# Optimization experiments

Hardware: AMD Instinct MI355X
Metric: run time of the kernel (lower is better)

## Reference

```python
import jax, jax.numpy as jnp
import numpy as np

B, S, D, E, F = 2, 2048, 1024, 14, 2048


def setup_inputs() -> dict:
    key = jax.random.key(0)
    k = jax.random.split(key, 4)
    h = jax.random.normal(k[0], (B, S, D), dtype=jnp.float32)
    router_w = jax.random.normal(k[1], (D, E), dtype=jnp.float32) * 0.02
    # kaiming-uniform-like scale for expert weights
    w1 = jax.random.uniform(k[2], (E, D, F), dtype=jnp.float32,
                            minval=-1.0, maxval=1.0) * float(np.sqrt(6.0 / D))
    w2 = jax.random.uniform(k[3], (E, F, D), dtype=jnp.float32,
                            minval=-1.0, maxval=1.0) * float(np.sqrt(6.0 / F))
    b1 = jnp.zeros((E, F), dtype=jnp.float32)
    b2 = jnp.zeros((E, D), dtype=jnp.float32)
    return {"h": h, "router_w": router_w, "w1": w1, "b1": b1, "w2": w2, "b2": b2}


def reference(h, router_w, w1, b1, w2, b2):
    Bb, Ss, Dd = h.shape
    x = h.reshape(-1, Dd)                                  # (N, D)
    logits = x @ router_w                                  # (N, E)
    assignments = jnp.argmax(logits, axis=-1)              # (N,) phase B routing
    probs = jax.nn.softmax(logits, axis=-1)
    weights = jnp.take_along_axis(probs, assignments[:, None], axis=1)[:, 0]  # (N,)
    # dense all-expert FFN (as in the original module)
    hid = jnp.einsum('nd,edf->nef', x, w1) + b1            # (N, E, F)
    hid = jax.nn.gelu(hid, approximate=False)
    all_out = jnp.einsum('nef,efd->ned', hid, w2) + b2     # (N, E, D)
    sel = jnp.take_along_axis(all_out, assignments[:, None, None], axis=1)[:, 0, :]
    moe_out = (sel * weights[:, None]).reshape(Bb, Ss, Dd)
    return moe_out
```

## Files before the change

kernel.cpp:

```cpp
#include <hip/hip_runtime.h>
#include <hip/hip_bf16.h>


#define NTOK 4096
#define NEXP 14
#define DDIM 1024
#define FDIM 2048

typedef __attribute__((ext_vector_type(8))) short short8;
typedef __attribute__((ext_vector_type(4))) float floatx4;

__device__ __forceinline__ unsigned bfr(float f) {
  unsigned u = __float_as_uint(f);
  return (u + 0x7FFFu + ((u >> 16) & 1u)) >> 16;
}
__device__ __forceinline__ unsigned pk2(float a, float b) {
  return bfr(a) | (bfr(b) << 16);
}

__device__ __forceinline__ void gload16(const void* g, void* l) {
  __builtin_amdgcn_global_load_lds((const __attribute__((address_space(1))) void*)g,
                                   (__attribute__((address_space(3))) void*)l, 16, 0, 0);
}

__global__ void k_init(const float* __restrict__ rw, float* __restrict__ rwT) {
  int i = blockIdx.x * 256 + threadIdx.x;
  if (i < DDIM * NEXP) rwT[(i % NEXP) * DDIM + i / NEXP] = rw[i];
}

__global__ __launch_bounds__(256) void k_router(
    const float* __restrict__ x, const float* __restrict__ rwT,
    int* __restrict__ assign, float* __restrict__ wgt,
    unsigned short* __restrict__ h16) {
  int wid = threadIdx.x >> 6, lane = threadIdx.x & 63;
  int n = blockIdx.x * 4 + wid;
  const float* xr = x + (size_t)n * DDIM;
  unsigned short* hr = h16 + (size_t)n * DDIM;
  double acc[NEXP];
#pragma unroll
  for (int e = 0; e < NEXP; e++) acc[e] = 0.0;
#pragma unroll
  for (int i = 0; i < 4; i++) {
    int d0 = i * 256 + lane * 4;
    float4 xv = *(const float4*)(xr + d0);
    uint2 hb;
    hb.x = pk2(xv.x, xv.y);
    hb.y = pk2(xv.z, xv.w);
    *(uint2*)(hr + d0) = hb;
    double x0 = xv.x, x1 = xv.y, x2 = xv.z, x3 = xv.w;
#pragma unroll
    for (int e = 0; e < NEXP; e++) {
      float4 rv = *(const float4*)(rwT + e * DDIM + d0);
      acc[e] += x0 * (double)rv.x + x1 * (double)rv.y + x2 * (double)rv.z + x3 * (double)rv.w;
    }
  }
#pragma unroll
  for (int e = 0; e < NEXP; e++)
    for (int m = 32; m > 0; m >>= 1) acc[e] += __shfl_xor(acc[e], m, 64);
  int best = 0;
  double bv = acc[0];
#pragma unroll
  for (int e = 1; e < NEXP; e++)
    if (acc[e] > bv) { bv = acc[e]; best = e; }
  float s = 0.f;
#pragma unroll
  for (int e = 0; e < NEXP; e++) s += expf((float)(acc[e] - bv));
  if (lane == 0) {
    wgt[n] = 1.0f / s;
    assign[n] = best;
  }
}

__global__ __launch_bounds__(1024) void k_sort(
    const int* __restrict__ assign, int* __restrict__ cnt,
    int* __restrict__ list, int* __restrict__ tiles, int* __restrict__ ntl) {
  __shared__ int clds[64][NEXP];
  __shared__ int tot[16];
  __shared__ int tstart[NEXP + 1];
  int tid = threadIdx.x;
  int wv = tid >> 6, lane = tid & 63;
  unsigned long long below = (1ull << lane) - 1ull;
  int e4[4], r4[4];
#pragma unroll
  for (int t = 0; t < 4; t++) {
    int n = wv * 256 + t * 64 + lane;
    int e = assign[n];
    int rank = 0, gcnt = 0;
#pragma unroll
    for (int xx = 0; xx < NEXP; xx++) {
      unsigned long long m = __ballot(e == xx);
      if (e == xx) rank = __popcll(m & below);
      if (lane == xx) gcnt = __popcll(m);
    }
    e4[t] = e;
    r4[t] = rank;
    if (lane < NEXP) clds[wv * 4 + t][lane] = gcnt;
  }
  __syncthreads();
  if (wv < NEXP) {
    int v = clds[lane][wv];
    int s = v;
    for (int m = 1; m < 64; m <<= 1) {
      int t = __shfl_up(s, m, 64);
      if (lane >= m) s += t;
    }
    clds[lane][wv] = s - v;
    if (lane == 63) {
      cnt[wv] = s;
      tot[wv] = s;
    }
  }
  __syncthreads();
#pragma unroll
  for (int t = 0; t < 4; t++) {
    int n = wv * 256 + t * 64 + lane;
    int e = e4[t];
    int pos = clds[wv * 4 + t][e] + r4[t];
    list[e * NTOK + pos] = n;
  }
  if (wv == 15) {
    int c = (lane < NEXP) ? tot[lane] : 0;
    int nt = (c + 127) >> 7;
    int st = nt;
    for (int m = 1; m < 64; m <<= 1) {
      int t = __shfl_up(st, m, 64);
      if (lane >= m) st += t;
    }
    if (lane < NEXP) tstart[lane] = st - nt;
    if (lane == NEXP - 1) {
      tstart[NEXP] = st;
      *ntl = st;
    }
    int totT = __shfl(st, NEXP - 1, 64);
    if (lane < totT) {
      int e = 0;
      while (tstart[e + 1] <= lane) e++;
      tiles[2 * lane] = e;
      tiles[2 * lane + 1] = (lane - tstart[e]) * 128;
    }
  }
}

__global__ __launch_bounds__(256) void k_prep(const float* __restrict__ W,
                                              unsigned short* __restrict__ img,
                                              int K, int N) {
  __shared__ float t32[4096];
  int KB = K >> 6, NB = N >> 6, K4 = KB >> 2;
  int b = blockIdx.x;
  int kb4 = b % K4;
  int nb_ = b / K4;
  int nblk = nb_ % NB, e = nb_ / NB;
  int t = threadIdx.x;
  int k = t >> 4, n4 = (t & 15) * 4;
  for (int z = 0; z < 4; z++) {
    int kblk = kb4 * 4 + z;
    const float* src = W + (size_t)e * K * N + (size_t)(kblk * 64) * N + nblk * 64;
#pragma unroll
    for (int j = 0; j < 4; j++) {
      int kk = k + j * 16;
      float4 v = *(const float4*)(src + (size_t)kk * N + n4);
      int sw = kk & 31;
      t32[kk * 64 + ((n4 + 0) ^ sw)] = v.x;
      t32[kk * 64 + ((n4 + 1) ^ sw)] = v.y;
      t32[kk * 64 + ((n4 + 2) ^ sw)] = v.z;
      t32[kk * 64 + ((n4 + 3) ^ sw)] = v.w;
    }
    __syncthreads();
    unsigned short* dst = img + (size_t)((e * NB + nblk) * KB + kblk) * 4096;
#pragma unroll
    for (int c = 0; c < 2; c++) {
      int ci = t + c * 256;
      int col = ci >> 3, q = ci & 7, k8 = q ^ (col & 7);
      float f[8];
#pragma unroll
      for (int j = 0; j < 8; j++) {
        int kk = k8 * 8 + j;
        f[j] = t32[kk * 64 + (col ^ (kk & 31))];
      }
      uint4 o;
      o.x = pk2(f[0], f[1]);
      o.y = pk2(f[2], f[3]);
      o.z = pk2(f[4], f[5]);
      o.w = pk2(f[6], f[7]);
      *(uint4*)(dst + ci * 8) = o;
    }
    __syncthreads();
  }
}

template <int LAYER>
__global__ __launch_bounds__(256, 3) void k_gemm_img(
    const unsigned short* __restrict__ Xb, const unsigned short* __restrict__ img,
    const float* __restrict__ Bias, const float* __restrict__ wgt,
    unsigned short* __restrict__ outB, float* __restrict__ outF,
    const int* __restrict__ wsI, const int* __restrict__ list) {
  constexpr int K = (LAYER == 1) ? DDIM : FDIM;
  constexpr int N = (LAYER == 1) ? FDIM : DDIM;
  constexpr int NIT = K / 64;
  constexpr int KB = K / 64, NB = N / 64;

  const int* cnt = wsI;
  const int* ntl = wsI + 48;
  const int* tiles = wsI + 64;

  int tI = blockIdx.y;
  if (tI >= *ntl) return;
  int e = tiles[2 * tI], m0 = tiles[2 * tI + 1];
  int rows = cnt[e] - m0;
  int base = e * NTOK + m0;
  int n0 = blockIdx.x * 64;

  __shared__ char sA[2][16384];
  __shared__ char sB[2][8192];
  __shared__ int tokL[128];
  __shared__ float wgtL[128];

  int tid = threadIdx.x;
  if (tid < 128) {
    int tok = list[base + tid] & (NTOK - 1);
    tokL[tid] = tok;
    if (LAYER == 2) wgtL[tid] = wgt[tok];
  }
  __syncthreads();

  int lane = tid & 63, wid = tid >> 6, wm = wid >> 1, wn = wid & 1;

  const char* gA[4];
  {
    unsigned sw = (unsigned)(((lane & 7) * 16) ^ ((lane >> 3) << 4));
#pragma unroll
    for (int j = 0; j < 4; j++) {
      int row = wid * 32 + j * 8 + (lane >> 3);
      gA[j] = (const char*)(Xb + (size_t)tokL[row] * K) + sw;
    }
  }
  const char* gB = (const char*)img +
                   (size_t)((e * NB + (n0 >> 6)) * KB) * 8192 + wid * 2048 + lane * 16;

  floatx4 acc[4][2];
#pragma unroll
  for (int i = 0; i < 4; i++)
#pragma unroll
    for (int j = 0; j < 2; j++) acc[i][j] = (floatx4){0.f, 0.f, 0.f, 0.f};

#define GLOAD_AB(it, p)                                                     \
  do {                                                                      \
    _Pragma("unroll") for (int j = 0; j < 4; j++)                           \
        gload16(gA[j] + (size_t)(it) * 128, sA[p] + (wid * 4 + j) * 1024);  \
    _Pragma("unroll") for (int j = 0; j < 2; j++)                           \
        gload16(gB + (size_t)(it) * 8192 + j * 1024,                        \
                sB[p] + wid * 2048 + j * 1024);                             \
  } while (0)

#define MFMA_PHASE(P)                                                                    \
  do {                                                                                   \
    const char* A_ = sA[P];                                                              \
    const char* B_ = sB[P];                                                              \
    _Pragma("unroll") for (int kc = 0; kc < 2; kc++) {                                   \
      short8 af[4], bf[2];                                                               \
      int kb = kc * 64 + ((lane >> 4) << 4);                                             \
      _Pragma("unroll") for (int f = 0; f < 4; f++) {                                    \
        int rr = wm * 64 + f * 16 + (lane & 15);                                         \
        af[f] = *(const short8*)(A_ + rr * 128 + (kb ^ ((rr & 7) << 4)));                \
      }                                                                                  \
      _Pragma("unroll") for (int f = 0; f < 2; f++) {                                    \
        int cc = wn * 32 + f * 16 + (lane & 15);                                         \
        bf[f] = *(const short8*)(B_ + cc * 128 + (kb ^ ((cc & 7) << 4)));                \
      }                                                                                  \
      _Pragma("unroll") for (int fm = 0; fm < 4; fm++)                                   \
      _Pragma("unroll") for (int fn = 0; fn < 2; fn++)                                   \
          acc[fm][fn] =                                                                  \
              __builtin_amdgcn_mfma_f32_16x16x32_bf16(af[fm], bf[fn], acc[fm][fn], 0, 0, 0); \
    }                                                                                    \
  } while (0)

  GLOAD_AB(0, 0);
  for (int it = 0; it < NIT - 1; ++it) {
    int p = it & 1;
    __builtin_amdgcn_sched_barrier(0);
    __builtin_amdgcn_s_barrier();
    GLOAD_AB(it + 1, p ^ 1);
    __builtin_amdgcn_sched_barrier(0);
    asm volatile("s_waitcnt vmcnt(6)" ::: "memory");
    __builtin_amdgcn_s_barrier();
    __builtin_amdgcn_sched_barrier(0);
    MFMA_PHASE(p);
  }
  {
    int p = (NIT - 1) & 1;
    __builtin_amdgcn_sched_barrier(0);
    __builtin_amdgcn_s_barrier();
    asm volatile("s_waitcnt vmcnt(0)" ::: "memory");
    __builtin_amdgcn_s_barrier();
    __builtin_amdgcn_sched_barrier(0);
    MFMA_PHASE(p);
  }
#undef GLOAD_AB
#undef MFMA_PHASE

  float bv[2];
#pragma unroll
  for (int f = 0; f < 2; f++) bv[f] = Bias[(size_t)e * N + n0 + wn * 32 + f * 16 + (lane & 15)];
#pragma unroll
  for (int fm = 0; fm < 4; fm++) {
#pragma unroll
    for (int r = 0; r < 4; r++) {
      int gr = wm * 64 + fm * 16 + ((lane >> 4) << 2) + r;
      if (gr < rows) {
        int tok = tokL[gr];
#pragma unroll
        for (int fn = 0; fn < 2; fn++) {
          int col = n0 + wn * 32 + fn * 16 + (lane & 15);
          float v = acc[fm][fn][r] + bv[fn];
          if (LAYER == 1) {
            v = 0.5f * v * (1.0f + erff(v * 0.70710678118654752f));
            outB[(size_t)tok * FDIM + col] = (unsigned short)bfr(v);
          } else {
            outF[(size_t)tok * DDIM + col] = v * wgtL[gr];
          }
        }
      }
    }
  }
}

extern "C" void kernel_launch(void* const* d_in, const int* in_sizes, int n_in,
                              void* d_out, int out_size, void* d_ws, size_t ws_size,
                              hipStream_t stream) {
  const float* h  = (const float*)d_in[0];
  const float* rw = (const float*)d_in[1];
  const float* w1 = (const float*)d_in[2];
  const float* b1 = (const float*)d_in[3];
  const float* w2 = (const float*)d_in[4];
  const float* b2 = (const float*)d_in[5];
  float* out = (float*)d_out;

  int* wsI = (int*)d_ws;
  int* assign = wsI + 160;
  float* wgt = (float*)(wsI + 4256);
  int* list = (int*)((char*)d_ws + 65536);
  float* rwT = (float*)((char*)d_ws + 294912);
  unsigned short* hid  = (unsigned short*)((char*)d_ws + 393216);
  unsigned short* h16  = (unsigned short*)((char*)d_ws + 17170432);
  unsigned short* img1 = (unsigned short*)((char*)d_ws + 25559040);
  unsigned short* img2 = (unsigned short*)((char*)d_ws + 17170432);

  k_init<<<56, 256, 0, stream>>>(rw, rwT);
  k_router<<<NTOK / 4, 256, 0, stream>>>(h, rwT, assign, wgt, h16);
  k_sort<<<1, 1024, 0, stream>>>(assign, wsI, list, wsI + 64, wsI + 48);
  k_prep<<<NEXP * (FDIM / 64) * (DDIM / 64 / 4), 256, 0, stream>>>(w1, img1, DDIM, FDIM);
  k_gemm_img<1><<<dim3(FDIM / 64, 45), 256, 0, stream>>>(h16, img1, b1, nullptr, hid, nullptr, wsI, list);
  k_prep<<<NEXP * (DDIM / 64) * (FDIM / 64 / 4), 256, 0, stream>>>(w2, img2, FDIM, DDIM);
  k_gemm_img<2><<<dim3(DDIM / 64, 45), 256, 0, stream>>>(hid, img2, b2, wgt, nullptr, out, wsI, list);
}
```

Baseline: 188.6 us.

## Co-schedule weight prep with router and layer-1 GEMM via fused launches

Merges the w1 bf16 image prep into the router launch and the w2 image prep into the layer-1 GEMM launch, using block-index ranges to dispatch each block to one body. The aim is to overlap the bandwidth-bound weight conversion with other work and to cut the number of launches. img2 moves to its own workspace region so it no longer aliases h16 while layer 1 still reads h16. In exchange the fused kernels carry the larger shared-memory footprint and the GEMM's register budget, which can lower occupancy for the prep blocks.

```diff
diff --git a/kernel.cpp b/kernel.cpp
--- a/kernel.cpp
+++ b/kernel.cpp
@@ -23,17 +23,28 @@
                                    (__attribute__((address_space(3))) void*)l, 16, 0, 0);
 }
 
+struct GemmSh {
+  char sA[2][16384];
+  char sB[2][8192];
+  int tokL[128];
+  float wgtL[128];
+};
+union FuseSh {
+  GemmSh g;
+  float t32[4096];
+};
+
 __global__ void k_init(const float* __restrict__ rw, float* __restrict__ rwT) {
   int i = blockIdx.x * 256 + threadIdx.x;
   if (i < DDIM * NEXP) rwT[(i % NEXP) * DDIM + i / NEXP] = rw[i];
 }
 
-__global__ __launch_bounds__(256) void k_router(
-    const float* __restrict__ x, const float* __restrict__ rwT,
+__device__ __forceinline__ void router_body(
+    int bid, const float* __restrict__ x, const float* __restrict__ rwT,
     int* __restrict__ assign, float* __restrict__ wgt,
     unsigned short* __restrict__ h16) {
   int wid = threadIdx.x >> 6, lane = threadIdx.x & 63;
-  int n = blockIdx.x * 4 + wid;
+  int n = bid * 4 + wid;
   const float* xr = x + (size_t)n * DDIM;
   unsigned short* hr = h16 + (size_t)n * DDIM;
   double acc[NEXP];
@@ -71,82 +82,11 @@
   }
 }
 
-__global__ __launch_bounds__(1024) void k_sort(
-    const int* __restrict__ assign, int* __restrict__ cnt,
-    int* __restrict__ list, int* __restrict__ tiles, int* __restrict__ ntl) {
-  __shared__ int clds[64][NEXP];
-  __shared__ int tot[16];
-  __shared__ int tstart[NEXP + 1];
-  int tid = threadIdx.x;
-  int wv = tid >> 6, lane = tid & 63;
-  unsigned long long below = (1ull << lane) - 1ull;
-  int e4[4], r4[4];
-#pragma unroll
-  for (int t = 0; t < 4; t++) {
-    int n = wv * 256 + t * 64 + lane;
-    int e = assign[n];
-    int rank = 0, gcnt = 0;
-#pragma unroll
-    for (int xx = 0; xx < NEXP; xx++) {
-      unsigned long long m = __ballot(e == xx);
-      if (e == xx) rank = __popcll(m & below);
-      if (lane == xx) gcnt = __popcll(m);
-    }
-    e4[t] = e;
-    r4[t] = rank;
-    if (lane < NEXP) clds[wv * 4 + t][lane] = gcnt;
-  }
-  __syncthreads();
-  if (wv < NEXP) {
-    int v = clds[lane][wv];
-    int s = v;
-    for (int m = 1; m < 64; m <<= 1) {
-      int t = __shfl_up(s, m, 64);
-      if (lane >= m) s += t;
-    }
-    clds[lane][wv] = s - v;
-    if (lane == 63) {
-      cnt[wv] = s;
-      tot[wv] = s;
-    }
-  }
-  __syncthreads();
-#pragma unroll
-  for (int t = 0; t < 4; t++) {
-    int n = wv * 256 + t * 64 + lane;
-    int e = e4[t];
-    int pos = clds[wv * 4 + t][e] + r4[t];
-    list[e * NTOK + pos] = n;
-  }
-  if (wv == 15) {
-    int c = (lane < NEXP) ? tot[lane] : 0;
-    int nt = (c + 127) >> 7;
-    int st = nt;
-    for (int m = 1; m < 64; m <<= 1) {
-      int t = __shfl_up(st, m, 64);
-      if (lane >= m) st += t;
-    }
-    if (lane < NEXP) tstart[lane] = st - nt;
-    if (lane == NEXP - 1) {
-      tstart[NEXP] = st;
-      *ntl = st;
-    }
-    int totT = __shfl(st, NEXP - 1, 64);
-    if (lane < totT) {
-      int e = 0;
-      while (tstart[e + 1] <= lane) e++;
-      tiles[2 * lane] = e;
-      tiles[2 * lane + 1] = (lane - tstart[e]) * 128;
-    }
-  }
-}
-
-__global__ __launch_bounds__(256) void k_prep(const float* __restrict__ W,
-                                              unsigned short* __restrict__ img,
-                                              int K, int N) {
-  __shared__ float t32[4096];
+__device__ __forceinline__ void prep_body(float* __restrict__ t32,
+                                          const float* __restrict__ W,
+                                          unsigned short* __restrict__ img,
+                                          int K, int N, int b) {
   int KB = K >> 6, NB = N >> 6, K4 = KB >> 2;
-  int b = blockIdx.x;
   int kb4 = b % K4;
   int nb_ = b / K4;
   int nblk = nb_ % NB, e = nb_ / NB;
@@ -189,7 +129,8 @@
 }
 
 template <int LAYER>
-__global__ __launch_bounds__(256, 3) void k_gemm_img(
+__device__ __forceinline__ void gemm_body(
+    GemmSh* sh, int tI, int n0,
     const unsigned short* __restrict__ Xb, const unsigned short* __restrict__ img,
     const float* __restrict__ Bias, const float* __restrict__ wgt,
     unsigned short* __restrict__ outB, float* __restrict__ outF,
@@ -203,17 +144,15 @@
   const int* ntl = wsI + 48;
   const int* tiles = wsI + 64;
 
-  int tI = blockIdx.y;
   if (tI >= *ntl) return;
   int e = tiles[2 * tI], m0 = tiles[2 * tI + 1];
   int rows = cnt[e] - m0;
   int base = e * NTOK + m0;
-  int n0 = blockIdx.x * 64;
-
-  __shared__ char sA[2][16384];
-  __shared__ char sB[2][8192];
-  __shared__ int tokL[128];
-  __shared__ float wgtL[128];
+
+  char (*sA)[16384] = sh->sA;
+  char (*sB)[8192] = sh->sB;
+  int* tokL = sh->tokL;
+  float* wgtL = sh->wgtL;
 
   int tid = threadIdx.x;
   if (tid < 128) {
@@ -324,6 +263,115 @@
   }
 }
 
+__global__ __launch_bounds__(256) void k_fuseA(
+    const float* __restrict__ x, const float* __restrict__ rwT,
+    int* __restrict__ assign, float* __restrict__ wgt,
+    unsigned short* __restrict__ h16,
+    const float* __restrict__ w1, unsigned short* __restrict__ img1) {
+  __shared__ float t32[4096];
+  int bid = blockIdx.x;
+  if (bid < NTOK / 4) {
+    router_body(bid, x, rwT, assign, wgt, h16);
+  } else {
+    prep_body(t32, w1, img1, DDIM, FDIM, bid - NTOK / 4);
+  }
+}
+
+__global__ __launch_bounds__(1024) void k_sort(
+    const int* __restrict__ assign, int* __restrict__ cnt,
+    int* __restrict__ list, int* __restrict__ tiles, int* __restrict__ ntl) {
+  __shared__ int clds[64][NEXP];
+  __shared__ int tot[16];
+  __shared__ int tstart[NEXP + 1];
+  int tid = threadIdx.x;
+  int wv = tid >> 6, lane = tid & 63;
+  unsigned long long below = (1ull << lane) - 1ull;
+  int e4[4], r4[4];
+#pragma unroll
+  for (int t = 0; t < 4; t++) {
+    int n = wv * 256 + t * 64 + lane;
+    int e = assign[n];
+    int rank = 0, gcnt = 0;
+#pragma unroll
+    for (int xx = 0; xx < NEXP; xx++) {
+      unsigned long long m = __ballot(e == xx);
+      if (e == xx) rank = __popcll(m & below);
+      if (lane == xx) gcnt = __popcll(m);
+    }
+    e4[t] = e;
+    r4[t] = rank;
+    if (lane < NEXP) clds[wv * 4 + t][lane] = gcnt;
+  }
+  __syncthreads();
+  if (wv < NEXP) {
+    int v = clds[lane][wv];
+    int s = v;
+    for (int m = 1; m < 64; m <<= 1) {
+      int t = __shfl_up(s, m, 64);
+      if (lane >= m) s += t;
+    }
+    clds[lane][wv] = s - v;
+    if (lane == 63) {
+      cnt[wv] = s;
+      tot[wv] = s;
+    }
+  }
+  __syncthreads();
+#pragma unroll
+  for (int t = 0; t < 4; t++) {
+    int n = wv * 256 + t * 64 + lane;
+    int e = e4[t];
+    int pos = clds[wv * 4 + t][e] + r4[t];
+    list[e * NTOK + pos] = n;
+  }
+  if (wv == 15) {
+    int c = (lane < NEXP) ? tot[lane] : 0;
+    int nt = (c + 127) >> 7;
+    int st = nt;
+    for (int m = 1; m < 64; m <<= 1) {
+      int t = __shfl_up(st, m, 64);
+      if (lane >= m) st += t;
+    }
+    if (lane < NEXP) tstart[lane] = st - nt;
+    if (lane == NEXP - 1) {
+      tstart[NEXP] = st;
+      *ntl = st;
+    }
+    int totT = __shfl(st, NEXP - 1, 64);
+    if (lane < totT) {
+      int e = 0;
+      while (tstart[e + 1] <= lane) e++;
+      tiles[2 * lane] = e;
+      tiles[2 * lane + 1] = (lane - tstart[e]) * 128;
+    }
+  }
+}
+
+__global__ __launch_bounds__(256, 3) void k_fuseB(
+    const unsigned short* __restrict__ h16, const unsigned short* __restrict__ img1,
+    const float* __restrict__ b1, unsigned short* __restrict__ hid,
+    const int* __restrict__ wsI, const int* __restrict__ list,
+    const float* __restrict__ w2, unsigned short* __restrict__ img2) {
+  __shared__ FuseSh sh;
+  int bid = blockIdx.x;
+  if (bid < (FDIM / 64) * 45) {
+    gemm_body<1>(&sh.g, bid >> 5, (bid & 31) << 6, h16, img1, b1, nullptr, hid,
+                 nullptr, wsI, list);
+  } else {
+    prep_body(sh.t32, w2, img2, FDIM, DDIM, bid - (FDIM / 64) * 45);
+  }
+}
+
+__global__ __launch_bounds__(256, 3) void k_gemm2(
+    const unsigned short* __restrict__ hid, const unsigned short* __restrict__ img2,
+    const float* __restrict__ b2, const float* __restrict__ wgt,
+    float* __restrict__ outF, const int* __restrict__ wsI,
+    const int* __restrict__ list) {
+  __shared__ GemmSh sh;
+  gemm_body<2>(&sh, blockIdx.y, blockIdx.x << 6, hid, img2, b2, wgt, nullptr,
+               outF, wsI, list);
+}
+
 extern "C" void kernel_launch(void* const* d_in, const int* in_sizes, int n_in,
                               void* d_out, int out_size, void* d_ws, size_t ws_size,
                               hipStream_t stream) {
@@ -343,13 +391,11 @@
   unsigned short* hid  = (unsigned short*)((char*)d_ws + 393216);
   unsigned short* h16  = (unsigned short*)((char*)d_ws + 17170432);
   unsigned short* img1 = (unsigned short*)((char*)d_ws + 25559040);
-  unsigned short* img2 = (unsigned short*)((char*)d_ws + 17170432);
+  unsigned short* img2 = (unsigned short*)((char*)d_ws + 54919168);
 
   k_init<<<56, 256, 0, stream>>>(rw, rwT);
-  k_router<<<NTOK / 4, 256, 0, stream>>>(h, rwT, assign, wgt, h16);
+  k_fuseA<<<NTOK / 4 + 1792, 256, 0, stream>>>(h, rwT, assign, wgt, h16, w1, img1);
   k_sort<<<1, 1024, 0, stream>>>(assign, wsI, list, wsI + 64, wsI + 48);
-  k_prep<<<NEXP * (FDIM / 64) * (DDIM / 64 / 4), 256, 0, stream>>>(w1, img1, DDIM, FDIM);
-  k_gemm_img<1><<<dim3(FDIM / 64, 45), 256, 0, stream>>>(h16, img1, b1, nullptr, hid, nullptr, wsI, list);
-  k_prep<<<NEXP * (DDIM / 64) * (FDIM / 64 / 4), 256, 0, stream>>>(w2, img2, FDIM, DDIM);
-  k_gemm_img<2><<<dim3(DDIM / 64, 45), 256, 0, stream>>>(hid, img2, b2, wgt, nullptr, out, wsI, list);
-}
+  k_fuseB<<<1440 + 1792, 256, 0, stream>>>(h16, img1, b1, hid, wsI, list, w2, img2);
+  k_gemm2<<<dim3(DDIM / 64, 45), 256, 0, stream>>>(hid, img2, b2, wgt, out, wsI, list);
+}
```

Result: faster. 167.1 us (-11.4%).
